# Optimization experiments

Hardware: AMD Instinct MI355X
Metric: run time of the kernel (lower is better)

The kernel has to match this reference:

```python
import jax, jax.numpy as jnp
import numpy as np

B, T, D_MODEL, HEAD_DIM = 8, 2048, 1024, 128


def setup_inputs() -> dict:
    key = jax.random.key(0)
    k1, k2, k3, k4 = jax.random.split(key, 4)
    scale = 1.0 / np.sqrt(D_MODEL)
    return {
        "x": jax.random.normal(k1, (B, T, D_MODEL), dtype=jnp.float32),
        "Wq": jax.random.normal(k2, (HEAD_DIM, D_MODEL), dtype=jnp.float32) * scale,
        "Wk": jax.random.normal(k3, (HEAD_DIM, D_MODEL), dtype=jnp.float32) * scale,
        "Wv": jax.random.normal(k4, (HEAD_DIM, D_MODEL), dtype=jnp.float32) * scale,
    }


def reference(x, Wq, Wk, Wv) -> jnp.ndarray:
    # x: [B, T, C]; torch Linear(no bias): y = x @ W.T, W: [head_dim, d_model]
    q = jnp.einsum("btc,hc->bth", x, Wq)  # [B, T, H]
    k = jnp.einsum("btc,hc->bth", x, Wk)
    v = jnp.einsum("btc,hc->bth", x, Wv)
    head_dim = Wq.shape[0]
    scores = jnp.einsum("bqh,bkh->bqk", q, k) / jnp.sqrt(jnp.float32(head_dim))  # [B, T, T]
    T_ = x.shape[1]
    causal = jnp.tril(jnp.ones((T_, T_), dtype=bool))
    scores = jnp.where(causal, scores, -jnp.inf)
    probs = jax.nn.softmax(scores, axis=-1)
    # dropout is identity at inference (eval mode)
    out = jnp.einsum("bqk,bkh->bqh", probs, v)  # [B, T, head_dim]
    return out
```

## Files before the change

kernel.cpp:

```cpp
#include <hip/hip_runtime.h>
#include <hip/hip_bf16.h>
#include <math.h>

#define T_ 2048
#define C_ 1024
#define H_ 128
#define NB 8
#define WN 131072
#define SC 0.08838834764831845f

typedef __attribute__((ext_vector_type(8))) short bf16x8;
typedef __attribute__((ext_vector_type(8))) unsigned short u16x8;
typedef __attribute__((ext_vector_type(4))) float f32x4;

#define MFMA16(a,b,c) __builtin_amdgcn_mfma_f32_16x16x32_bf16((a),(b),(c),0,0,0)

__device__ __forceinline__ unsigned short f2bf(float f) {
    union { float f; unsigned u; } v; v.f = f;
    unsigned r = v.u + 0x7fffu + ((v.u >> 16) & 1u);
    return (unsigned short)(r >> 16);
}
__device__ __forceinline__ float bf2f(unsigned short u) {
    union { unsigned u; float f; } v; v.u = ((unsigned)u) << 16; return v.f;
}
__device__ __forceinline__ unsigned pk2bf(float a, float b) {
    __hip_bfloat162 h = __float22bfloat162_rn(float2{a, b});
    union { __hip_bfloat162 h; unsigned u; } v; v.h = h; return v.u;
}
__device__ __forceinline__ void gld16(void* lds, const void* g) {
    __builtin_amdgcn_global_load_lds(
        (const __attribute__((address_space(1))) unsigned*)g,
        (__attribute__((address_space(3))) unsigned*)lds, 16, 0, 0);
}

__global__ __launch_bounds__(256) void wconv(const float* __restrict__ Wq,
                                             const float* __restrict__ Wk,
                                             const float* __restrict__ Wv,
                                             unsigned short* __restrict__ Wb) {
    int e = (blockIdx.x * 256 + threadIdx.x) * 8;
    int which = e >> 17;
    int off = e & (WN - 1);
    const float* src = (which == 0) ? Wq : (which == 1 ? Wk : Wv);
    float s = (which == 0) ? SC : 1.0f;
    const float4* p = (const float4*)(src + off);
    float4 a = p[0], b = p[1];
    uint4 o = { pk2bf(a.x * s, a.y * s), pk2bf(a.z * s, a.w * s),
                pk2bf(b.x * s, b.y * s), pk2bf(b.z * s, b.w * s) };
    *(uint4*)(Wb + e) = o;
}

__global__ __launch_bounds__(256, 2) void proj(const float* __restrict__ x,
                                               const unsigned short* __restrict__ Wb,
                                               unsigned short* __restrict__ Q,
                                               unsigned short* __restrict__ K,
                                               unsigned short* __restrict__ V) {
    __shared__ unsigned short Xs[2][64][64];
    __shared__ unsigned short Ws[2][192][64];

    const int tid  = threadIdx.x;
    const int wave = tid >> 6, lane = tid & 63;
    const int quad = lane >> 4, l16 = lane & 15;
    const int wm   = wave >> 1, wn = wave & 1;
    const int m0   = (blockIdx.x >> 1) * 64;
    const int n0   = (blockIdx.x & 1) * 192;

    f32x4 acc[2][6];
    #pragma unroll
    for (int i = 0; i < 2; i++)
        #pragma unroll
        for (int j = 0; j < 6; j++) acc[i][j] = {0.f, 0.f, 0.f, 0.f};

    const int xrow = tid >> 2, xcg = tid & 3;
    const float* xg = x + (size_t)(m0 + xrow) * C_ + xcg * 16;
    const int xk = xrow & 7;
    const unsigned short* wg = Wb + (size_t)(n0 + wave * 48 + (lane >> 3)) * C_
                               + (size_t)(((lane & 7) ^ (lane >> 3)) * 8);

    float4 xr0, xr1, xr2, xr3;
    #define ISSUE(buf, kc) do {                                                   \
        _Pragma("unroll")                                                         \
        for (int i = 0; i < 6; i++)                                               \
            gld16(&Ws[buf][wave * 48 + i * 8][0], wg + (size_t)i * 8 * C_ + (kc));\
        const float* xp = xg + (kc);                                              \
        xr0 = *(const float4*)xp;        xr1 = *(const float4*)(xp + 4);          \
        xr2 = *(const float4*)(xp + 8);  xr3 = *(const float4*)(xp + 12);         \
    } while (0)

    #define XWRITE(buf) do {                                                      \
        uint4 u0 = { pk2bf(xr0.x, xr0.y), pk2bf(xr0.z, xr0.w),                    \
                     pk2bf(xr1.x, xr1.y), pk2bf(xr1.z, xr1.w) };                  \
        uint4 u1 = { pk2bf(xr2.x, xr2.y), pk2bf(xr2.z, xr2.w),                    \
                     pk2bf(xr3.x, xr3.y), pk2bf(xr3.z, xr3.w) };                  \
        *(uint4*)&Xs[buf][xrow][((2 * xcg)     ^ xk) * 8] = u0;                   \
        *(uint4*)&Xs[buf][xrow][((2 * xcg + 1) ^ xk) * 8] = u1;                   \
    } while (0)

    ISSUE(0, 0);
    XWRITE(0);
    for (int it = 0; it < 16; it++) {
        __syncthreads();
        const int buf = it & 1;
        if (it < 15) ISSUE(buf ^ 1, (it + 1) * 64);
        const int key = l16 & 7;
        bf16x8 af[2][2];
        #pragma unroll
        for (int kk = 0; kk < 2; kk++)
            #pragma unroll
            for (int mf = 0; mf < 2; mf++)
                af[mf][kk] = *(bf16x8*)&Xs[buf][wm * 32 + mf * 16 + l16]
                                          [((kk * 4 + quad) ^ key) * 8];
        #pragma unroll
        for (int kk = 0; kk < 2; kk++)
            #pragma unroll
            for (int nf = 0; nf < 6; nf++) {
                bf16x8 bq = *(bf16x8*)&Ws[buf][wn * 96 + nf * 16 + l16]
                                         [((kk * 4 + quad) ^ key) * 8];
                acc[0][nf] = MFMA16(af[0][kk], bq, acc[0][nf]);
                acc[1][nf] = MFMA16(af[1][kk], bq, acc[1][nf]);
            }
        if (it < 15) XWRITE(buf ^ 1);
    }
    #undef ISSUE
    #undef XWRITE

    #pragma unroll
    for (int nf = 0; nf < 6; nf++) {
        int nb = n0 + wn * 96 + nf * 16;
        int which = nb >> 7;
        unsigned short* dst = (which == 0) ? Q : (which == 1 ? K : V);
        int c = (nb & 127) + l16;
        #pragma unroll
        for (int mf = 0; mf < 2; mf++)
            #pragma unroll
            for (int r = 0; r < 4; r++)
                dst[(size_t)(m0 + wm * 32 + mf * 16 + quad * 4 + r) * H_ + c] = f2bf(acc[mf][nf][r]);
    }
}

__global__ __launch_bounds__(256, 3) void attn(const unsigned short* __restrict__ Qg,
                                               const unsigned short* __restrict__ Kg,
                                               const unsigned short* __restrict__ Vg,
                                               unsigned short* __restrict__ Ob,
                                               float* __restrict__ Ml) {
    const int bx = blockIdx.x;
    const int s  = bx & 7, qt = 31 - (bx >> 3);
    const int b  = blockIdx.y;
    const int qbase = qt * 64, kstart = s * 256;
    if (kstart > qbase) return;
    const int kend  = (kstart + 256 < qbase + 64) ? kstart + 256 : qbase + 64;
    const int niter = (kend - kstart) >> 6;

    __shared__ unsigned short Ks[4][64][32];
    __shared__ unsigned short Vt[128 * 64];
    __shared__ unsigned short Ps[4][16][64];

    const int tid = threadIdx.x, wave = tid >> 6, lane = tid & 63;
    const int quad = lane >> 4, l16 = lane & 15;
    const size_t base = (size_t)b * T_ * H_;

    const unsigned short* ksrc = Kg + base + (size_t)(kstart + (lane >> 2)) * H_ + wave * 32 + (lane & 3) * 8;
    #pragma unroll
    for (int p = 0; p < 4; p++) gld16(&Ks[wave][p * 16][0], ksrc + (size_t)p * 16 * H_);
    const unsigned short* vsrc = Vg + base + (size_t)(kstart + wave * 8 + quad * 2) * H_ + l16 * 8;
    u16x8 vr[2][2];
    vr[0][0] = *(const u16x8*)vsrc;             vr[0][1] = *(const u16x8*)(vsrc + H_);
    vr[1][0] = *(const u16x8*)(vsrc + 32 * H_); vr[1][1] = *(const u16x8*)(vsrc + 33 * H_);

    bf16x8 qf[4];
    const unsigned short* qp = Qg + base + (size_t)(qbase + wave * 16 + l16) * H_ + quad * 8;
    #pragma unroll
    for (int kk = 0; kk < 4; kk++) qf[kk] = *(const bf16x8*)(qp + kk * 32);

    f32x4 o[8];
    #pragma unroll
    for (int i = 0; i < 8; i++) o[i] = {0.f, 0.f, 0.f, 0.f};
    float m_i = -INFINITY, l_i = 0.f;
    const int swz = (l16 & 7) << 3;
    const int qg = qbase + wave * 16 + l16;

    __syncthreads();

    #pragma unroll
    for (int g = 0; g < 2; g++) {
        int t0 = wave * 8 + g * 32 + quad * 2;
        int t8 = t0 >> 3;
        #pragma unroll
        for (int j = 0; j < 8; j++) {
            int h = l16 * 8 + j;
            unsigned pk = (unsigned)(unsigned short)vr[g][0][j] | ((unsigned)(unsigned short)vr[g][1][j] << 16);
            int blk = (t8 ^ (h & 7) ^ ((h >> 3) & 7)) & 7;
            *(unsigned*)&Vt[h * 64 + blk * 8 + (t0 & 7)] = pk;
        }
    }

    for (int kt = 0; ; kt++) {
        const int kbase = kstart + kt * 64;
        f32x4 st[4];
        #pragma unroll
        for (int nf = 0; nf < 4; nf++) st[nf] = {0.f, 0.f, 0.f, 0.f};
        #pragma unroll
        for (int kk = 0; kk < 4; kk++)
            #pragma unroll
            for (int nf = 0; nf < 4; nf++) {
                bf16x8 kfr = *(bf16x8*)&Ks[kk][nf * 16 + l16][quad * 8];
                st[nf] = MFMA16(kfr, qf[kk], st[nf]);
            }
        if (kbase + 64 > qbase) {
            #pragma unroll
            for (int nf = 0; nf < 4; nf++) {
                int kg = kbase + nf * 16 + quad * 4;
                #pragma unroll
                for (int r = 0; r < 4; r++)
                    if (kg + r > qg) st[nf][r] = -INFINITY;
            }
        }
        float mx = st[0][0];
        #pragma unroll
        for (int nf = 0; nf < 4; nf++)
            #pragma unroll
            for (int r = 0; r < 4; r++) mx = fmaxf(mx, st[nf][r]);
        mx = fmaxf(mx, __shfl_xor(mx, 16, 64));
        mx = fmaxf(mx, __shfl_xor(mx, 32, 64));
        float mnew = fmaxf(m_i, mx);
        float al = __expf(m_i - mnew);
        m_i = mnew;
        float rs = 0.f;
        #pragma unroll
        for (int nf = 0; nf < 4; nf++)
            #pragma unroll
            for (int r = 0; r < 4; r++) {
                float e = __expf(st[nf][r] - mnew);
                st[nf][r] = e; rs += e;
            }
        rs += __shfl_xor(rs, 16, 64);
        rs += __shfl_xor(rs, 32, 64);
        l_i = al * l_i + rs;
        #pragma unroll
        for (int nf = 0; nf < 4; nf++) {
            uint2 pk = { pk2bf(st[nf][0], st[nf][1]), pk2bf(st[nf][2], st[nf][3]) };
            *(uint2*)&Ps[wave][l16][(nf * 16 + quad * 4) ^ swz] = pk;
        }
        float a0 = __shfl(al, quad * 4 + 0, 64), a1 = __shfl(al, quad * 4 + 1, 64);
        float a2 = __shfl(al, quad * 4 + 2, 64), a3 = __shfl(al, quad * 4 + 3, 64);
        #pragma unroll
        for (int i = 0; i < 8; i++) {
            o[i][0] *= a0; o[i][1] *= a1; o[i][2] *= a2; o[i][3] *= a3;
        }
        __syncthreads();

        const bool more = (kt + 1 < niter);
        if (more) {
            ksrc += 64 * H_;
            #pragma unroll
            for (int p = 0; p < 4; p++) gld16(&Ks[wave][p * 16][0], ksrc + (size_t)p * 16 * H_);
            vsrc += 64 * H_;
            vr[0][0] = *(const u16x8*)vsrc;             vr[0][1] = *(const u16x8*)(vsrc + H_);
            vr[1][0] = *(const u16x8*)(vsrc + 32 * H_); vr[1][1] = *(const u16x8*)(vsrc + 33 * H_);
        }
        bf16x8 pa0 = *(bf16x8*)&Ps[wave][l16][(quad * 8) ^ swz];
        bf16x8 pa1 = *(bf16x8*)&Ps[wave][l16][(32 + quad * 8) ^ swz];
        #pragma unroll
        for (int nf = 0; nf < 8; nf++) {
            int h = nf * 16 + l16;
            int ex = (h & 7) ^ ((h >> 3) & 7);
            bf16x8 v0 = *(bf16x8*)&Vt[h * 64 + ((quad ^ ex) & 7) * 8];
            bf16x8 v1 = *(bf16x8*)&Vt[h * 64 + (((quad + 4) ^ ex) & 7) * 8];
            o[nf] = MFMA16(pa0, v0, o[nf]);
            o[nf] = MFMA16(pa1, v1, o[nf]);
        }
        if (!more) break;
        __syncthreads();
        #pragma unroll
        for (int g = 0; g < 2; g++) {
            int t0 = wave * 8 + g * 32 + quad * 2;
            int t8 = t0 >> 3;
            #pragma unroll
            for (int j = 0; j < 8; j++) {
                int h = l16 * 8 + j;
                unsigned pk = (unsigned)(unsigned short)vr[g][0][j] | ((unsigned)(unsigned short)vr[g][1][j] << 16);
                int blk = (t8 ^ (h & 7) ^ ((h >> 3) & 7)) & 7;
                *(unsigned*)&Vt[h * 64 + blk * 8 + (t0 & 7)] = pk;
            }
        }
    }

    const int g2 = qt >> 2;
    const int Pq = 2 * g2 * (g2 + 1) + (qt & 3) * (g2 + 1);
    const int slot = (Pq + s) * NB + b;
    float lq[4];
    #pragma unroll
    for (int r = 0; r < 4; r++) lq[r] = __shfl(l_i, quad * 4 + r, 64);
    const size_t obase = (size_t)slot * 64 * 128;
    #pragma unroll
    for (int r = 0; r < 4; r++) {
        float invl = 1.0f / lq[r];
        #pragma unroll
        for (int nf = 0; nf < 8; nf++)
            Ob[obase + (size_t)(wave * 16 + quad * 4 + r) * 128 + nf * 16 + l16] = f2bf(o[nf][r] * invl);
    }
    if (lane < 16) {
        int ridx = slot * 64 + wave * 16 + l16;
        Ml[ridx * 2]     = m_i;
        Ml[ridx * 2 + 1] = l_i;
    }
}

__global__ __launch_bounds__(256) void merge(const unsigned short* __restrict__ Ob,
                                             const float* __restrict__ Ml,
                                             float* __restrict__ out) {
    const int qt = blockIdx.x, b = blockIdx.y;
    const int g = qt >> 2;
    const int Pq = 2 * g * (g + 1) + (qt & 3) * (g + 1);
    const int ns = g + 1;
    const int tid = threadIdx.x;
    const int row = tid >> 2, c0 = (tid & 3) * 32;

    float mv[8], lv[8], mg = -INFINITY;
    for (int s2 = 0; s2 < ns; s2++) {
        int slot = (Pq + s2) * NB + b;
        mv[s2] = Ml[(slot * 64 + row) * 2];
        lv[s2] = Ml[(slot * 64 + row) * 2 + 1];
        mg = fmaxf(mg, mv[s2]);
    }
    float L = 0.f, w[8];
    for (int s2 = 0; s2 < ns; s2++) { w[s2] = lv[s2] * __expf(mv[s2] - mg); L += w[s2]; }
    float inv = 1.0f / L;

    float accv[32];
    #pragma unroll
    for (int i = 0; i < 32; i++) accv[i] = 0.f;
    for (int s2 = 0; s2 < ns; s2++) {
        int slot = (Pq + s2) * NB + b;
        const unsigned short* op = Ob + ((size_t)(slot * 64 + row)) * 128 + c0;
        #pragma unroll
        for (int cc = 0; cc < 4; cc++) {
            u16x8 v = *(const u16x8*)(op + cc * 8);
            #pragma unroll
            for (int j = 0; j < 8; j++) accv[cc * 8 + j] += w[s2] * bf2f(v[j]);
        }
    }
    float* od = out + ((size_t)(b * T_ + qt * 64 + row)) * 128 + c0;
    #pragma unroll
    for (int cc = 0; cc < 8; cc++) {
        float4 w4 = { accv[cc*4] * inv, accv[cc*4+1] * inv, accv[cc*4+2] * inv, accv[cc*4+3] * inv };
        *(float4*)(od + cc * 4) = w4;
    }
}

extern "C" void kernel_launch(void* const* d_in, const int* in_sizes, int n_in,
                              void* d_out, int out_size, void* d_ws, size_t ws_size,
                              hipStream_t stream) {
    const float* x  = (const float*)d_in[0];
    const float* Wq = (const float*)d_in[1];
    const float* Wk = (const float*)d_in[2];
    const float* Wv = (const float*)d_in[3];

    char* ws = (char*)d_ws;
    unsigned short* Wb = (unsigned short*)ws;
    unsigned short* Q  = (unsigned short*)(ws + (size_t) 1 * (1u << 20));
    unsigned short* K  = (unsigned short*)(ws + (size_t) 5 * (1u << 20));
    unsigned short* V  = (unsigned short*)(ws + (size_t) 9 * (1u << 20));
    unsigned short* Ob = (unsigned short*)(ws + (size_t)13 * (1u << 20));
    float*          Ml = (float*)(ws + (size_t)32 * (1u << 20));
    float* out = (float*)d_out;

    hipLaunchKernelGGL(wconv, dim3(192), dim3(256), 0, stream, Wq, Wk, Wv, Wb);
    hipLaunchKernelGGL(proj,  dim3(512), dim3(256), 0, stream, x, Wb, Q, K, V);
    hipLaunchKernelGGL(attn,  dim3(256, NB), dim3(256), 0, stream, Q, K, V, Ob, Ml);
    hipLaunchKernelGGL(merge, dim3(32, NB), dim3(256), 0, stream, Ob, Ml, out);
}
```

Measured before the change: 175.0 us.

## Load K fragments directly from global and double-buffer transposed V in LDS

The attention kernel no longer stages K tiles in shared memory. Each wave loads its K MFMA fragments straight from global (L2) memory, and the transposed V tile is double-buffered so one barrier per iteration is removed. It also raises launch_bounds occupancy from 3 to 4 blocks and wraps the MFMA sections in s_setprio. The aim is to cut LDS traffic and synchronisation, at the cost of redundant global K reads across waves that may add latency.

```diff
diff --git a/kernel.cpp b/kernel.cpp
--- a/kernel.cpp
+++ b/kernel.cpp
@@ -137,7 +137,7 @@
     }
 }
 
-__global__ __launch_bounds__(256, 3) void attn(const unsigned short* __restrict__ Qg,
+__global__ __launch_bounds__(256, 4) void attn(const unsigned short* __restrict__ Qg,
                                                const unsigned short* __restrict__ Kg,
                                                const unsigned short* __restrict__ Vg,
                                                unsigned short* __restrict__ Ob,
@@ -150,17 +150,13 @@
     const int kend  = (kstart + 256 < qbase + 64) ? kstart + 256 : qbase + 64;
     const int niter = (kend - kstart) >> 6;
 
-    __shared__ unsigned short Ks[4][64][32];
-    __shared__ unsigned short Vt[128 * 64];
+    __shared__ unsigned short Vt[2][128 * 64];
     __shared__ unsigned short Ps[4][16][64];
 
     const int tid = threadIdx.x, wave = tid >> 6, lane = tid & 63;
     const int quad = lane >> 4, l16 = lane & 15;
     const size_t base = (size_t)b * T_ * H_;
 
-    const unsigned short* ksrc = Kg + base + (size_t)(kstart + (lane >> 2)) * H_ + wave * 32 + (lane & 3) * 8;
-    #pragma unroll
-    for (int p = 0; p < 4; p++) gld16(&Ks[wave][p * 16][0], ksrc + (size_t)p * 16 * H_);
     const unsigned short* vsrc = Vg + base + (size_t)(kstart + wave * 8 + quad * 2) * H_ + l16 * 8;
     u16x8 vr[2][2];
     vr[0][0] = *(const u16x8*)vsrc;             vr[0][1] = *(const u16x8*)(vsrc + H_);
@@ -171,6 +167,8 @@
     #pragma unroll
     for (int kk = 0; kk < 4; kk++) qf[kk] = *(const bf16x8*)(qp + kk * 32);
 
+    const unsigned short* kp = Kg + base + (size_t)(kstart + l16) * H_ + quad * 8;
+
     f32x4 o[8];
     #pragma unroll
     for (int i = 0; i < 8; i++) o[i] = {0.f, 0.f, 0.f, 0.f};
@@ -178,33 +176,44 @@
     const int swz = (l16 & 7) << 3;
     const int qg = qbase + wave * 16 + l16;
 
+    #define VTWRITE(bufi) do {                                                       \
+        _Pragma("unroll")                                                            \
+        for (int g = 0; g < 2; g++) {                                                \
+            int t0 = wave * 8 + g * 32 + quad * 2;                                   \
+            int t8 = t0 >> 3;                                                        \
+            _Pragma("unroll")                                                        \
+            for (int j = 0; j < 8; j++) {                                            \
+                int h = l16 * 8 + j;                                                 \
+                unsigned pk = (unsigned)(unsigned short)vr[g][0][j]                  \
+                            | ((unsigned)(unsigned short)vr[g][1][j] << 16);         \
+                int blk = (t8 ^ (h & 7) ^ ((h >> 3) & 7)) & 7;                       \
+                *(unsigned*)&Vt[bufi][h * 64 + blk * 8 + (t0 & 7)] = pk;             \
+            }                                                                        \
+        }                                                                            \
+    } while (0)
+
+    VTWRITE(0);
     __syncthreads();
-
-    #pragma unroll
-    for (int g = 0; g < 2; g++) {
-        int t0 = wave * 8 + g * 32 + quad * 2;
-        int t8 = t0 >> 3;
-        #pragma unroll
-        for (int j = 0; j < 8; j++) {
-            int h = l16 * 8 + j;
-            unsigned pk = (unsigned)(unsigned short)vr[g][0][j] | ((unsigned)(unsigned short)vr[g][1][j] << 16);
-            int blk = (t8 ^ (h & 7) ^ ((h >> 3) & 7)) & 7;
-            *(unsigned*)&Vt[h * 64 + blk * 8 + (t0 & 7)] = pk;
-        }
-    }
 
     for (int kt = 0; ; kt++) {
         const int kbase = kstart + kt * 64;
+        const int buf = kt & 1;
         f32x4 st[4];
         #pragma unroll
         for (int nf = 0; nf < 4; nf++) st[nf] = {0.f, 0.f, 0.f, 0.f};
-        #pragma unroll
-        for (int kk = 0; kk < 4; kk++)
-            #pragma unroll
-            for (int nf = 0; nf < 4; nf++) {
-                bf16x8 kfr = *(bf16x8*)&Ks[kk][nf * 16 + l16][quad * 8];
-                st[nf] = MFMA16(kfr, qf[kk], st[nf]);
-            }
+        const unsigned short* kq = kp + (size_t)kt * 64 * H_;
+        __builtin_amdgcn_s_setprio(1);
+        #pragma unroll
+        for (int kk = 0; kk < 4; kk++) {
+            bf16x8 kfr[4];
+            #pragma unroll
+            for (int nf = 0; nf < 4; nf++)
+                kfr[nf] = *(const bf16x8*)(kq + (size_t)(nf * 16) * H_ + kk * 32);
+            #pragma unroll
+            for (int nf = 0; nf < 4; nf++)
+                st[nf] = MFMA16(kfr[nf], qf[kk], st[nf]);
+        }
+        __builtin_amdgcn_s_setprio(0);
         if (kbase + 64 > qbase) {
             #pragma unroll
             for (int nf = 0; nf < 4; nf++) {
@@ -240,49 +249,36 @@
             uint2 pk = { pk2bf(st[nf][0], st[nf][1]), pk2bf(st[nf][2], st[nf][3]) };
             *(uint2*)&Ps[wave][l16][(nf * 16 + quad * 4) ^ swz] = pk;
         }
-        float a0 = __shfl(al, quad * 4 + 0, 64), a1 = __shfl(al, quad * 4 + 1, 64);
-        float a2 = __shfl(al, quad * 4 + 2, 64), a3 = __shfl(al, quad * 4 + 3, 64);
-        #pragma unroll
-        for (int i = 0; i < 8; i++) {
-            o[i][0] *= a0; o[i][1] *= a1; o[i][2] *= a2; o[i][3] *= a3;
-        }
-        __syncthreads();
-
         const bool more = (kt + 1 < niter);
         if (more) {
-            ksrc += 64 * H_;
-            #pragma unroll
-            for (int p = 0; p < 4; p++) gld16(&Ks[wave][p * 16][0], ksrc + (size_t)p * 16 * H_);
             vsrc += 64 * H_;
             vr[0][0] = *(const u16x8*)vsrc;             vr[0][1] = *(const u16x8*)(vsrc + H_);
             vr[1][0] = *(const u16x8*)(vsrc + 32 * H_); vr[1][1] = *(const u16x8*)(vsrc + 33 * H_);
         }
+        float a0 = __shfl(al, quad * 4 + 0, 64), a1 = __shfl(al, quad * 4 + 1, 64);
+        float a2 = __shfl(al, quad * 4 + 2, 64), a3 = __shfl(al, quad * 4 + 3, 64);
+        #pragma unroll
+        for (int i = 0; i < 8; i++) {
+            o[i][0] *= a0; o[i][1] *= a1; o[i][2] *= a2; o[i][3] *= a3;
+        }
         bf16x8 pa0 = *(bf16x8*)&Ps[wave][l16][(quad * 8) ^ swz];
         bf16x8 pa1 = *(bf16x8*)&Ps[wave][l16][(32 + quad * 8) ^ swz];
+        __builtin_amdgcn_s_setprio(1);
         #pragma unroll
         for (int nf = 0; nf < 8; nf++) {
             int h = nf * 16 + l16;
             int ex = (h & 7) ^ ((h >> 3) & 7);
-            bf16x8 v0 = *(bf16x8*)&Vt[h * 64 + ((quad ^ ex) & 7) * 8];
-            bf16x8 v1 = *(bf16x8*)&Vt[h * 64 + (((quad + 4) ^ ex) & 7) * 8];
+            bf16x8 v0 = *(bf16x8*)&Vt[buf][h * 64 + ((quad ^ ex) & 7) * 8];
+            bf16x8 v1 = *(bf16x8*)&Vt[buf][h * 64 + (((quad + 4) ^ ex) & 7) * 8];
             o[nf] = MFMA16(pa0, v0, o[nf]);
             o[nf] = MFMA16(pa1, v1, o[nf]);
         }
+        __builtin_amdgcn_s_setprio(0);
         if (!more) break;
+        VTWRITE(buf ^ 1);
         __syncthreads();
-        #pragma unroll
-        for (int g = 0; g < 2; g++) {
-            int t0 = wave * 8 + g * 32 + quad * 2;
-            int t8 = t0 >> 3;
-            #pragma unroll
-            for (int j = 0; j < 8; j++) {
-                int h = l16 * 8 + j;
-                unsigned pk = (unsigned)(unsigned short)vr[g][0][j] | ((unsigned)(unsigned short)vr[g][1][j] << 16);
-                int blk = (t8 ^ (h & 7) ^ ((h >> 3) & 7)) & 7;
-                *(unsigned*)&Vt[h * 64 + blk * 8 + (t0 & 7)] = pk;
-            }
-        }
-    }
+    }
+    #undef VTWRITE
 
     const int g2 = qt >> 2;
     const int Pq = 2 * g2 * (g2 + 1) + (qt & 3) * (g2 + 1);
```

Measured after the change: 223.8 us. +27.9%, slower.
